# Performance work log

Hardware: AMD Instinct MI355X
Metric: run time of the kernel (lower is better)

Reference implementation:

```python
import jax, jax.numpy as jnp
import numpy as np

N_NODES = 50000
N_EDGES = 400000
N_GROUPS = 10000
N_GRAPHS = 256
IN_CH = 64
EDGE_DIM = 16
HID = 64
HEADS = 4
OUT_CH = 1


def segment_mean(vals, idx, n):
    s = jax.ops.segment_sum(vals, idx, num_segments=n)
    c = jax.ops.segment_sum(jnp.ones(idx.shape[0], vals.dtype), idx, num_segments=n)
    c = jnp.maximum(c, 1.0).reshape((n,) + (1,) * (vals.ndim - 1))
    return s / c


def gatv2(x, src, dst, wl, wr, att, bias, edge_attr=None, we=None):
    # PyG GATv2Conv (concat=True, negative_slope=0.2, add_self_loops=True,
    # fill_value='mean', share_weights=False).
    N = x.shape[0]
    H, C = att.shape
    loop = jnp.arange(N, dtype=src.dtype)
    s = jnp.concatenate([src, loop])
    d = jnp.concatenate([dst, loop])
    dc = jnp.minimum(d, N - 1)  # clamp dummy (masked) targets for gathers
    xl = (x @ wl).reshape(N, H, C)  # source transform
    xr = (x @ wr).reshape(N, H, C)  # target transform
    m = xl[s] + xr[dc]  # [E+N, H, C]
    if edge_attr is not None:
        loop_attr = segment_mean(edge_attr, dst, N)  # self-loop attr = mean of incoming
        e = jnp.concatenate([edge_attr, loop_attr], axis=0) @ we
        m = m + e.reshape(-1, H, C)
    score = jnp.sum(jax.nn.leaky_relu(m, 0.2) * att, axis=-1)  # [E+N, H]
    smax = jax.ops.segment_max(score, d, num_segments=N)
    ex = jnp.exp(score - smax[dc])
    den = jax.ops.segment_sum(ex, d, num_segments=N)
    alpha = ex / den[dc]
    out = jax.ops.segment_sum(alpha[..., None] * xl[s], d, num_segments=N)
    return out.reshape(N, H * C) + bias


def setup_inputs() -> dict:
    key = jax.random.key(0)
    ks = jax.random.split(key, 32)
    p = lambda i, shape: jax.random.normal(ks[i], shape, jnp.float32) * 0.05
    x = jax.random.normal(ks[0], (N_NODES, IN_CH), jnp.float32)
    edge_index = jax.random.randint(ks[1], (2, N_EDGES), 0, N_NODES)
    edge_attr = jax.random.normal(ks[2], (N_EDGES, EDGE_DIM), jnp.float32)
    batch = (jnp.arange(N_NODES) * N_GRAPHS) // N_NODES
    pharma_index = (jnp.arange(N_NODES) * N_GROUPS) // N_NODES
    return dict(
        x=x, edge_index=edge_index, edge_attr=edge_attr, batch=batch,
        pharma_index=pharma_index, num_graphs=N_GRAPHS,
        w_edge=p(3, (EDGE_DIM, HID)), b_edge=jnp.zeros((HID,), jnp.float32),
        g1_wl=p(4, (IN_CH, HEADS * HID)), g1_wr=p(5, (IN_CH, HEADS * HID)),
        g1_att=p(6, (HEADS, HID)), g1_we=p(7, (HID, HEADS * HID)),
        g1_b=jnp.zeros((HEADS * HID,), jnp.float32),
        g2_wl=p(8, (HEADS * HID, HID)), g2_wr=p(9, (HEADS * HID, HID)),
        g2_att=p(10, (1, HID)), g2_we=p(11, (HID, HID)),
        g2_b=jnp.zeros((HID,), jnp.float32),
        g3_wl=p(12, (HID, HID)), g3_wr=p(13, (HID, HID)),
        g3_att=p(14, (1, HID)), g3_b=jnp.zeros((HID,), jnp.float32),
        g4_wl=p(15, (HID, HID)), g4_wr=p(16, (HID, HID)),
        g4_att=p(17, (1, HID)), g4_b=jnp.zeros((HID,), jnp.float32),
        w1=p(18, (HID, 64)), b1=jnp.zeros((64,), jnp.float32),
        w2=p(19, (64, OUT_CH)), b2=jnp.zeros((OUT_CH,), jnp.float32),
    )


def reference(x, edge_index, edge_attr, batch, pharma_index, num_graphs,
              w_edge, b_edge,
              g1_wl, g1_wr, g1_att, g1_we, g1_b,
              g2_wl, g2_wr, g2_att, g2_we, g2_b,
              g3_wl, g3_wr, g3_att, g3_b,
              g4_wl, g4_wr, g4_att, g4_b,
              w1, b1, w2, b2):
    src, dst = edge_index[0], edge_index[1]
    ea = edge_attr @ w_edge + b_edge  # edge_embed
    h = jax.nn.elu(gatv2(x, src, dst, g1_wl, g1_wr, g1_att, g1_b, ea, g1_we))
    h = jax.nn.elu(gatv2(h, src, dst, g2_wl, g2_wr, g2_att, g2_b, ea, g2_we))
    # pharmacophore pooling (scatter_mean)
    gx = segment_mean(h, pharma_index, N_GROUPS)
    rbatch = segment_mean(batch.astype(jnp.float32), pharma_index, N_GROUPS).astype(jnp.int32)
    # reduced-graph edges: map node edges to group indices, drop intra-group
    # self-edges by routing their target to a dummy segment N_GROUPS.
    sg = pharma_index[src]
    dg = pharma_index[dst]
    dg = jnp.where(sg != dg, dg, N_GROUPS)
    h = jax.nn.elu(gatv2(gx, sg, dg, g3_wl, g3_wr, g3_att, g3_b))
    h = jax.nn.elu(gatv2(h, sg, dg, g4_wl, g4_wr, g4_att, g4_b))
    h = segment_mean(h, rbatch, num_graphs)  # global_mean_pool
    h = jax.nn.relu(h @ w1 + b1)
    return h @ w2 + b2
```

## Files before the change

kernel.cpp:

```cpp
#include <hip/hip_runtime.h>
#include <cstdint>
#include <cstddef>

#define NN 50000
#define NE 400000
#define NG 10000
#define NBG 256

static inline int imin(int a, int b) { return a < b ? a : b; }

__device__ __forceinline__ float wave_sum64(float v) {
#pragma unroll
  for (int off = 32; off > 0; off >>= 1) v += __shfl_xor(v, off, 64);
  return v;
}

__device__ __forceinline__ float bcast_lane(float v, int k) {
  return __int_as_float(__builtin_amdgcn_readlane(__float_as_int(v), k));
}


__global__ void count_dst_kernel(const int* __restrict__ dst, int* __restrict__ cnt, int E) {
  int e = blockIdx.x * blockDim.x + threadIdx.x;
  if (e < E) atomicAdd(&cnt[dst[e]], 1);
}

__global__ void fill_node_kernel(const int* __restrict__ src, const int* __restrict__ dst,
                                 int* __restrict__ cursor, int* __restrict__ csr_src,
                                 int* __restrict__ csr_eid, int E) {
  int e = blockIdx.x * blockDim.x + threadIdx.x;
  if (e < E) {
    int pos = atomicAdd(&cursor[dst[e]], 1);
    csr_src[pos] = src[e];
    csr_eid[pos] = e;
  }
}

__global__ void count_grp_kernel(const int* __restrict__ src, const int* __restrict__ dst,
                                 const int* __restrict__ ph, int* __restrict__ cnt, int E) {
  int e = blockIdx.x * blockDim.x + threadIdx.x;
  if (e < E) {
    int sg = ph[src[e]], dg = ph[dst[e]];
    if (sg != dg) atomicAdd(&cnt[dg], 1);
  }
}

__global__ void fill_grp_kernel(const int* __restrict__ src, const int* __restrict__ dst,
                                const int* __restrict__ ph, int* __restrict__ cursor,
                                int* __restrict__ gsrc, int E) {
  int e = blockIdx.x * blockDim.x + threadIdx.x;
  if (e < E) {
    int sg = ph[src[e]], dg = ph[dst[e]];
    if (sg != dg) {
      int pos = atomicAdd(&cursor[dg], 1);
      gsrc[pos] = sg;
    }
  }
}

__global__ void exscan_block_kernel(const int* __restrict__ cnt, int* __restrict__ rowptr, int n) {
  __shared__ int wsum[16];
  int tid = threadIdx.x;
  int chunk = (n + 1023) >> 10;
  int s0 = tid * chunk;
  int s1 = s0 + chunk; if (s1 > n) s1 = n;
  int sum = 0;
  for (int i = s0; i < s1; i++) sum += cnt[i];
  int lane = tid & 63, w = tid >> 6;
  int v = sum, s = sum;
#pragma unroll
  for (int off = 1; off < 64; off <<= 1) {
    int t = __shfl_up(s, off);
    if (lane >= off) s += t;
  }
  if (lane == 63) wsum[w] = s;
  __syncthreads();
  if (tid == 0) {
    int c = 0;
#pragma unroll
    for (int i = 0; i < 16; i++) { int t = wsum[i]; wsum[i] = c; c += t; }
  }
  __syncthreads();
  int run = wsum[w] + (s - v);
  for (int i = s0; i < s1; i++) { rowptr[i] = run; run += cnt[i]; }
  if (tid == 1023) rowptr[n] = run;
}


__global__ void mean_attr_kernel(const int* __restrict__ rowptr, const int* __restrict__ csr_eid,
                                 const float* __restrict__ eattr, float* __restrict__ mattr, int N) {
  int t = blockIdx.x * blockDim.x + threadIdx.x;
  if (t >= N * 16) return;
  int n = t >> 4, k = t & 15;
  int e0 = rowptr[n], e1 = rowptr[n + 1];
  float s = 0.f;
  for (int p = e0; p < e1; p++) s += eattr[(size_t)csr_eid[p] * 16 + k];
  mattr[t] = (e1 > e0) ? s / (float)(e1 - e0) : 0.f;
}

__global__ void fuse_we_kernel(const float* __restrict__ w_edge, const float* __restrict__ b_edge,
                               const float* __restrict__ g1_we, const float* __restrict__ g2_we,
                               float* __restrict__ We2_1, float* __restrict__ be2_1,
                               float* __restrict__ We2_2, float* __restrict__ be2_2) {
  int t = blockIdx.x * blockDim.x + threadIdx.x;
  if (t < 16 * 256) {
    int k = t >> 8, j = t & 255;
    float s = 0.f;
    for (int c = 0; c < 64; c++) s += w_edge[k * 64 + c] * g1_we[c * 256 + j];
    We2_1[t] = s;
  } else if (t < 16 * 256 + 256) {
    int j = t - 16 * 256;
    float s = 0.f;
    for (int c = 0; c < 64; c++) s += b_edge[c] * g1_we[c * 256 + j];
    be2_1[j] = s;
  } else if (t < 16 * 256 + 256 + 16 * 64) {
    int u = t - (16 * 256 + 256);
    int k = u >> 6, j = u & 63;
    float s = 0.f;
    for (int c = 0; c < 64; c++) s += w_edge[k * 64 + c] * g2_we[c * 64 + j];
    We2_2[u] = s;
  } else if (t < 16 * 256 + 256 + 16 * 64 + 64) {
    int j = t - (16 * 256 + 256 + 16 * 64);
    float s = 0.f;
    for (int c = 0; c < 64; c++) s += b_edge[c] * g2_we[c * 64 + j];
    be2_2[j] = s;
  }
}

template <int IN, int OUT>
__global__ __launch_bounds__(256) void matvec_kernel(int nRows,
    const float* __restrict__ X, const float* __restrict__ W, float* __restrict__ Y) {
  constexpr int KT = IN / 64;
  const int lane = threadIdx.x & 63;
  const int wv = threadIdx.x >> 6;
  const int batch = blockIdx.x * 4 + wv;
  const int jc = blockIdx.y;
  const int row = batch * 64 + lane;
  const int rc = row < nRows ? row : nRows - 1;
  const float* xp = X + (size_t)rc * IN;
  float acc[64];
#pragma unroll
  for (int j = 0; j < 64; j++) acc[j] = 0.f;
  for (int kt = 0; kt < KT; kt++) {
    float xr[64];
#pragma unroll
    for (int q = 0; q < 16; q++) {
      const float4 v = *(const float4*)(xp + kt * 64 + q * 4);
      xr[q * 4 + 0] = v.x; xr[q * 4 + 1] = v.y; xr[q * 4 + 2] = v.z; xr[q * 4 + 3] = v.w;
    }
    const float* wb = W + (size_t)kt * 64 * OUT + jc * 64;
#pragma unroll
    for (int k = 0; k < 64; k++) {
#pragma unroll
      for (int j = 0; j < 64; j++) acc[j] += xr[k] * wb[(size_t)k * OUT + j];
    }
  }
  if (row < nRows) {
    float* yp = Y + (size_t)row * OUT + jc * 64;
#pragma unroll
    for (int q = 0; q < 16; q++) {
      float4 v;
      v.x = acc[q * 4 + 0]; v.y = acc[q * 4 + 1]; v.z = acc[q * 4 + 2]; v.w = acc[q * 4 + 3];
      *(float4*)(yp + q * 4) = v;
    }
  }
}

template <int H, bool HASE>
__global__ __launch_bounds__(256) void gat_kernel(
    int N,
    const int* __restrict__ rowptr,
    const int* __restrict__ csr_src,
    const int* __restrict__ csr_eid,
    const float* __restrict__ eattr,
    const float* __restrict__ mattr,
    const float* __restrict__ We2,
    const float* __restrict__ be2,
    const float* __restrict__ xl,
    const float* __restrict__ xr,
    const float* __restrict__ att,
    const float* __restrict__ bias,
    float* __restrict__ out)
{
  constexpr int F = H * 64;
  const int lane = threadIdx.x & 63;
  const int wv = threadIdx.x >> 6;

  float att_r[H], bias_r[H], be2_r[H], wreg[16 * H];
#pragma unroll
  for (int r = 0; r < H; r++) {
    att_r[r] = att[r * 64 + lane];
    bias_r[r] = bias[r * 64 + lane];
    be2_r[r] = 0.f;
  }
  if constexpr (HASE) {
#pragma unroll
    for (int r = 0; r < H; r++) be2_r[r] = be2[r * 64 + lane];
#pragma unroll
    for (int k = 0; k < 16; k++)
#pragma unroll
      for (int r = 0; r < H; r++) wreg[k * H + r] = We2[k * F + r * 64 + lane];
  }

  for (int n = blockIdx.x * 4 + wv; n < N; n += gridDim.x * 4) {
    const int e0 = rowptr[n], e1 = rowptr[n + 1];
    float xr_r[H], xls[H];
#pragma unroll
    for (int r = 0; r < H; r++) {
      xr_r[r] = xr[(size_t)n * F + r * 64 + lane];
      xls[r] = xl[(size_t)n * F + r * 64 + lane];
    }
    float ev[H];
#pragma unroll
    for (int r = 0; r < H; r++) ev[r] = 0.f;
    if constexpr (HASE) {
      if (e1 > e0) {
        float av = (lane < 16) ? mattr[(size_t)n * 16 + lane] : 0.f;
#pragma unroll
        for (int k = 0; k < 16; k++) {
          float a = bcast_lane(av, k);
#pragma unroll
          for (int r = 0; r < H; r++) ev[r] += a * wreg[k * H + r];
        }
#pragma unroll
        for (int r = 0; r < H; r++) ev[r] += be2_r[r];
      }
    }
    float m_run[H], den[H], acc[H];
#pragma unroll
    for (int r = 0; r < H; r++) {
      float vv = xls[r] + xr_r[r] + ev[r];
      vv = vv > 0.f ? vv : 0.2f * vv;
      float sc = wave_sum64(vv * att_r[r]);
      m_run[r] = sc; den[r] = 1.f; acc[r] = xls[r];
    }
    for (int pos = e0; pos < e1; pos++) {
      const int s = csr_src[pos];
      float ev2[H];
#pragma unroll
      for (int r = 0; r < H; r++) ev2[r] = 0.f;
      if constexpr (HASE) {
        const int eid = csr_eid[pos];
        float av = (lane < 16) ? eattr[(size_t)eid * 16 + lane] : 0.f;
#pragma unroll
        for (int k = 0; k < 16; k++) {
          float a = bcast_lane(av, k);
#pragma unroll
          for (int r = 0; r < H; r++) ev2[r] += a * wreg[k * H + r];
        }
#pragma unroll
        for (int r = 0; r < H; r++) ev2[r] += be2_r[r];
      }
      float xsr[H], sc[H];
#pragma unroll
      for (int r = 0; r < H; r++) xsr[r] = xl[(size_t)s * F + r * 64 + lane];
#pragma unroll
      for (int r = 0; r < H; r++) {
        float vv = xsr[r] + xr_r[r] + ev2[r];
        vv = vv > 0.f ? vv : 0.2f * vv;
        sc[r] = wave_sum64(vv * att_r[r]);
      }
#pragma unroll
      for (int r = 0; r < H; r++) {
        float mo = m_run[r];
        float mn = fmaxf(mo, sc[r]);
        float sa = __expf(mo - mn);
        float ex = __expf(sc[r] - mn);
        den[r] = den[r] * sa + ex;
        acc[r] = acc[r] * sa + ex * xsr[r];
        m_run[r] = mn;
      }
    }
#pragma unroll
    for (int r = 0; r < H; r++) {
      float o = acc[r] / den[r] + bias_r[r];
      out[(size_t)n * F + r * 64 + lane] = o > 0.f ? o : (__expf(o) - 1.f);
    }
  }
}


__global__ void pool_ph_scatter_kernel(const float* __restrict__ h, const int* __restrict__ ph,
                                       const int* __restrict__ batch, float* __restrict__ gsum,
                                       float* __restrict__ bsum, int* __restrict__ gcnt, int N) {
  int t = blockIdx.x * blockDim.x + threadIdx.x;
  if (t >= N * 64) return;
  int n = t >> 6, c = t & 63;
  int g = ph[n];
  atomicAdd(&gsum[(size_t)g * 64 + c], h[t]);
  if (c == 0) {
    atomicAdd(&gcnt[g], 1);
    atomicAdd(&bsum[g], (float)batch[n]);
  }
}

__global__ void pool_ph_final_kernel(const float* __restrict__ gsum, const float* __restrict__ bsum,
                                     const int* __restrict__ gcnt, float* __restrict__ gx,
                                     int* __restrict__ rbatch, int G) {
  int t = blockIdx.x * blockDim.x + threadIdx.x;
  if (t >= G * 64) return;
  int g = t >> 6, c = t & 63;
  float cn = fmaxf((float)gcnt[g], 1.f);
  gx[t] = gsum[t] / cn;
  if (c == 0) rbatch[g] = (int)(bsum[g] / cn);
}

__global__ void pool_graph_scatter_kernel(const float* __restrict__ h, const int* __restrict__ rbatch,
                                          float* __restrict__ psum, int* __restrict__ pcnt, int G) {
  int t = blockIdx.x * blockDim.x + threadIdx.x;
  if (t >= G * 64) return;
  int g = t >> 6, c = t & 63;
  int b = rbatch[g];
  atomicAdd(&psum[(size_t)b * 64 + c], h[t]);
  if (c == 0) atomicAdd(&pcnt[b], 1);
}

__global__ void pool_graph_final_kernel(const float* __restrict__ psum, const int* __restrict__ pcnt,
                                        float* __restrict__ pooled) {
  int t = blockIdx.x * blockDim.x + threadIdx.x;
  if (t >= NBG * 64) return;
  int b = t >> 6;
  pooled[t] = psum[t] / fmaxf((float)pcnt[b], 1.f);
}


__global__ void fc1_kernel(const float* __restrict__ pooled, const float* __restrict__ w1,
                           const float* __restrict__ b1, float* __restrict__ o) {
  int g = blockIdx.x, lane = threadIdx.x;
  float p = pooled[g * 64 + lane];
  float acc = b1[lane];
#pragma unroll 8
  for (int k = 0; k < 64; k++) acc += __shfl(p, k, 64) * w1[k * 64 + lane];
  o[g * 64 + lane] = fmaxf(acc, 0.f);
}

__global__ void fc2_kernel(const float* __restrict__ o1, const float* __restrict__ w2,
                           const float* __restrict__ b2, float* __restrict__ out) {
  int g = threadIdx.x;
  float acc = b2[0];
  for (int k = 0; k < 64; k++) acc += o1[g * 64 + k] * w2[k];
  out[g] = acc;
}


extern "C" void kernel_launch(void* const* d_in, const int* in_sizes, int n_in,
                              void* d_out, int out_size, void* d_ws, size_t ws_size,
                              hipStream_t stream) {
  (void)in_sizes; (void)n_in; (void)out_size; (void)ws_size;
  const float* x      = (const float*)d_in[0];
  const int*   eidx   = (const int*)d_in[1];
  const float* eattr  = (const float*)d_in[2];
  const int*   batch  = (const int*)d_in[3];
  const int*   ph     = (const int*)d_in[4];
  const float* w_edge = (const float*)d_in[6];
  const float* b_edge = (const float*)d_in[7];
  const float* g1_wl  = (const float*)d_in[8];
  const float* g1_wr  = (const float*)d_in[9];
  const float* g1_att = (const float*)d_in[10];
  const float* g1_we  = (const float*)d_in[11];
  const float* g1_b   = (const float*)d_in[12];
  const float* g2_wl  = (const float*)d_in[13];
  const float* g2_wr  = (const float*)d_in[14];
  const float* g2_att = (const float*)d_in[15];
  const float* g2_we  = (const float*)d_in[16];
  const float* g2_b   = (const float*)d_in[17];
  const float* g3_wl  = (const float*)d_in[18];
  const float* g3_wr  = (const float*)d_in[19];
  const float* g3_att = (const float*)d_in[20];
  const float* g3_b   = (const float*)d_in[21];
  const float* g4_wl  = (const float*)d_in[22];
  const float* g4_wr  = (const float*)d_in[23];
  const float* g4_att = (const float*)d_in[24];
  const float* g4_b   = (const float*)d_in[25];
  const float* w1     = (const float*)d_in[26];
  const float* b1     = (const float*)d_in[27];
  const float* w2     = (const float*)d_in[28];
  const float* b2     = (const float*)d_in[29];
  float* out = (float*)d_out;
  const int* src = eidx;
  const int* dst = eidx + NE;

  char* ws = (char*)d_ws;
  size_t off = 0;
  auto alloc = [&](size_t bytes) -> void* {
    size_t o = off;
    off = (off + bytes + 255) & ~(size_t)255;
    return (void*)(ws + o);
  };
  int*   rowptr  = (int*)alloc((NN + 1) * 4);
  int*   cursor  = (int*)alloc((NN + 1) * 4);
  int*   csr_src = (int*)alloc((size_t)NE * 4);
  int*   csr_eid = (int*)alloc((size_t)NE * 4);
  int*   growptr = (int*)alloc((NG + 1) * 4);
  int*   gcursor = (int*)alloc((NG + 1) * 4);
  int*   gsrc    = (int*)alloc((size_t)NE * 4);
  float* mattr   = (float*)alloc((size_t)NN * 16 * 4);
  float* We2_1   = (float*)alloc(16 * 256 * 4);
  float* be2_1   = (float*)alloc(256 * 4);
  float* We2_2   = (float*)alloc(16 * 64 * 4);
  float* be2_2   = (float*)alloc(64 * 4);
  float* xl1     = (float*)alloc((size_t)NN * 256 * 4);
  float* xr1     = (float*)alloc((size_t)NN * 256 * 4);
  float* h1      = (float*)alloc((size_t)NN * 256 * 4);
  float* bsum    = (float*)alloc(NG * 4);
  int*   gcnt    = (int*)alloc(NG * 4);
  int*   rbatch  = (int*)alloc(NG * 4);
  float* psum    = (float*)alloc(NBG * 64 * 4);
  int*   pcnt    = (int*)alloc(NBG * 4);
  float* pooled  = (float*)alloc(NBG * 64 * 4);
  float* fc1o    = (float*)alloc(NBG * 64 * 4);
  float* xl2 = xl1;
  float* xr2 = xl1 + (size_t)NN * 64;
  float* h2  = xl1 + (size_t)NN * 128;
  float* gsum = xr1;
  float* gx   = xr1 + (size_t)NG * 64 * 1;
  float* xl3  = xr1 + (size_t)NG * 64 * 2;
  float* xr3  = xr1 + (size_t)NG * 64 * 3;
  float* h3   = xr1 + (size_t)NG * 64 * 4;
  float* xl4  = xr1 + (size_t)NG * 64 * 5;
  float* xr4  = xr1 + (size_t)NG * 64 * 6;
  float* h4   = xr1 + (size_t)NG * 64 * 7;

  hipMemsetAsync(cursor, 0, (NN + 1) * 4, stream);
  count_dst_kernel<<<(NE + 255) / 256, 256, 0, stream>>>(dst, cursor, NE);
  exscan_block_kernel<<<1, 1024, 0, stream>>>(cursor, rowptr, NN);
  hipMemcpyAsync(cursor, rowptr, (NN + 1) * 4, hipMemcpyDeviceToDevice, stream);
  fill_node_kernel<<<(NE + 255) / 256, 256, 0, stream>>>(src, dst, cursor, csr_src, csr_eid, NE);
  mean_attr_kernel<<<(NN * 16 + 255) / 256, 256, 0, stream>>>(rowptr, csr_eid, eattr, mattr, NN);
  fuse_we_kernel<<<(16 * 256 + 256 + 16 * 64 + 64 + 255) / 256, 256, 0, stream>>>(
      w_edge, b_edge, g1_we, g2_we, We2_1, be2_1, We2_2, be2_2);

  {
    dim3 g1((NN + 255) / 256, 4);
    matvec_kernel<64, 256><<<g1, 256, 0, stream>>>(NN, x, g1_wl, xl1);
    matvec_kernel<64, 256><<<g1, 256, 0, stream>>>(NN, x, g1_wr, xr1);
  }
  int gatgrid = imin((NN + 3) / 4, 3072);
  gat_kernel<4, true><<<gatgrid, 256, 0, stream>>>(NN, rowptr, csr_src, csr_eid, eattr, mattr,
                                                   We2_1, be2_1, xl1, xr1, g1_att, g1_b, h1);
  {
    dim3 g2((NN + 255) / 256, 1);
    matvec_kernel<256, 64><<<g2, 256, 0, stream>>>(NN, h1, g2_wl, xl2);
    matvec_kernel<256, 64><<<g2, 256, 0, stream>>>(NN, h1, g2_wr, xr2);
  }
  gat_kernel<1, true><<<gatgrid, 256, 0, stream>>>(NN, rowptr, csr_src, csr_eid, eattr, mattr,
                                                   We2_2, be2_2, xl2, xr2, g2_att, g2_b, h2);

  hipMemsetAsync(gsum, 0, (size_t)NG * 64 * 4, stream);
  hipMemsetAsync(bsum, 0, NG * 4, stream);
  hipMemsetAsync(gcnt, 0, NG * 4, stream);
  pool_ph_scatter_kernel<<<(NN * 64 + 255) / 256, 256, 0, stream>>>(h2, ph, batch, gsum, bsum, gcnt, NN);
  pool_ph_final_kernel<<<(NG * 64 + 255) / 256, 256, 0, stream>>>(gsum, bsum, gcnt, gx, rbatch, NG);

  hipMemsetAsync(gcursor, 0, (NG + 1) * 4, stream);
  count_grp_kernel<<<(NE + 255) / 256, 256, 0, stream>>>(src, dst, ph, gcursor, NE);
  exscan_block_kernel<<<1, 1024, 0, stream>>>(gcursor, growptr, NG);
  hipMemcpyAsync(gcursor, growptr, (NG + 1) * 4, hipMemcpyDeviceToDevice, stream);
  fill_grp_kernel<<<(NE + 255) / 256, 256, 0, stream>>>(src, dst, ph, gcursor, gsrc, NE);

  int gatgrid2 = imin((NG + 3) / 4, 2560);
  {
    dim3 g3((NG + 255) / 256, 1);
    matvec_kernel<64, 64><<<g3, 256, 0, stream>>>(NG, gx, g3_wl, xl3);
    matvec_kernel<64, 64><<<g3, 256, 0, stream>>>(NG, gx, g3_wr, xr3);
    gat_kernel<1, false><<<gatgrid2, 256, 0, stream>>>(NG, growptr, gsrc, nullptr, nullptr, nullptr,
                                                       nullptr, nullptr, xl3, xr3, g3_att, g3_b, h3);
    matvec_kernel<64, 64><<<g3, 256, 0, stream>>>(NG, h3, g4_wl, xl4);
    matvec_kernel<64, 64><<<g3, 256, 0, stream>>>(NG, h3, g4_wr, xr4);
    gat_kernel<1, false><<<gatgrid2, 256, 0, stream>>>(NG, growptr, gsrc, nullptr, nullptr, nullptr,
                                                       nullptr, nullptr, xl4, xr4, g4_att, g4_b, h4);
  }

  hipMemsetAsync(psum, 0, NBG * 64 * 4, stream);
  hipMemsetAsync(pcnt, 0, NBG * 4, stream);
  pool_graph_scatter_kernel<<<(NG * 64 + 255) / 256, 256, 0, stream>>>(h4, rbatch, psum, pcnt, NG);
  pool_graph_final_kernel<<<(NBG * 64 + 255) / 256, 256, 0, stream>>>(psum, pcnt, pooled);
  fc1_kernel<<<NBG, 64, 0, stream>>>(pooled, w1, b1, fc1o);
  fc2_kernel<<<1, 256, 0, stream>>>(fc1o, w2, b2, out);
}
```

Measured before the change: 1.422 ms.

## Interleave head layout, pack CSR, pipeline edge loads and use DPP reductions in GAT

```diff
diff --git a/kernel.cpp b/kernel.cpp
--- a/kernel.cpp
+++ b/kernel.cpp
@@ -9,14 +9,18 @@
 
 static inline int imin(int a, int b) { return a < b ? a : b; }
 
-__device__ __forceinline__ float wave_sum64(float v) {
-#pragma unroll
-  for (int off = 32; off > 0; off >>= 1) v += __shfl_xor(v, off, 64);
-  return v;
-}
-
-__device__ __forceinline__ float bcast_lane(float v, int k) {
-  return __int_as_float(__builtin_amdgcn_readlane(__float_as_int(v), k));
+template <int CTRL>
+__device__ __forceinline__ float dpp_mov(float v) {
+  return __int_as_float(__builtin_amdgcn_update_dpp(0, __float_as_int(v), CTRL, 0xf, 0xf, true));
+}
+__device__ __forceinline__ float wave_sum_dpp(float v) {
+  v += dpp_mov<0x111>(v);
+  v += dpp_mov<0x112>(v);
+  v += dpp_mov<0x114>(v);
+  v += dpp_mov<0x118>(v);
+  v += dpp_mov<0x142>(v);
+  v += dpp_mov<0x143>(v);
+  return __int_as_float(__builtin_amdgcn_readlane(__float_as_int(v), 63));
 }
 
 
@@ -26,13 +30,11 @@
 }
 
 __global__ void fill_node_kernel(const int* __restrict__ src, const int* __restrict__ dst,
-                                 int* __restrict__ cursor, int* __restrict__ csr_src,
-                                 int* __restrict__ csr_eid, int E) {
+                                 int* __restrict__ cursor, int2* __restrict__ cpack, int E) {
   int e = blockIdx.x * blockDim.x + threadIdx.x;
   if (e < E) {
     int pos = atomicAdd(&cursor[dst[e]], 1);
-    csr_src[pos] = src[e];
-    csr_eid[pos] = e;
+    cpack[pos] = make_int2(src[e], e);
   }
 }
 
@@ -87,14 +89,14 @@
 }
 
 
-__global__ void mean_attr_kernel(const int* __restrict__ rowptr, const int* __restrict__ csr_eid,
+__global__ void mean_attr_kernel(const int* __restrict__ rowptr, const int2* __restrict__ cpack,
                                  const float* __restrict__ eattr, float* __restrict__ mattr, int N) {
   int t = blockIdx.x * blockDim.x + threadIdx.x;
   if (t >= N * 16) return;
   int n = t >> 4, k = t & 15;
   int e0 = rowptr[n], e1 = rowptr[n + 1];
   float s = 0.f;
-  for (int p = e0; p < e1; p++) s += eattr[(size_t)csr_eid[p] * 16 + k];
+  for (int p = e0; p < e1; p++) s += eattr[(size_t)cpack[p].y * 16 + k];
   mattr[t] = (e1 > e0) ? s / (float)(e1 - e0) : 0.f;
 }
 
@@ -127,51 +129,128 @@
   }
 }
 
-template <int IN, int OUT>
+template <int IN, int OUT, bool TR>
 __global__ __launch_bounds__(256) void matvec_kernel(int nRows,
     const float* __restrict__ X, const float* __restrict__ W, float* __restrict__ Y) {
-  constexpr int KT = IN / 64;
   const int lane = threadIdx.x & 63;
   const int wv = threadIdx.x >> 6;
-  const int batch = blockIdx.x * 4 + wv;
-  const int jc = blockIdx.y;
-  const int row = batch * 64 + lane;
+  const int row = (blockIdx.x * 4 + wv) * 64 + lane;
   const int rc = row < nRows ? row : nRows - 1;
   const float* xp = X + (size_t)rc * IN;
-  float acc[64];
-#pragma unroll
-  for (int j = 0; j < 64; j++) acc[j] = 0.f;
-  for (int kt = 0; kt < KT; kt++) {
-    float xr[64];
+  if constexpr (TR) {
+    static_assert(IN == 64, "TR path assumes IN==64");
+    constexpr int H = OUT / 64;
+    float xt[64];
 #pragma unroll
     for (int q = 0; q < 16; q++) {
-      const float4 v = *(const float4*)(xp + kt * 64 + q * 4);
-      xr[q * 4 + 0] = v.x; xr[q * 4 + 1] = v.y; xr[q * 4 + 2] = v.z; xr[q * 4 + 3] = v.w;
-    }
-    const float* wb = W + (size_t)kt * 64 * OUT + jc * 64;
-#pragma unroll
-    for (int k = 0; k < 64; k++) {
-#pragma unroll
-      for (int j = 0; j < 64; j++) acc[j] += xr[k] * wb[(size_t)k * OUT + j];
-    }
-  }
-  if (row < nRows) {
-    float* yp = Y + (size_t)row * OUT + jc * 64;
-#pragma unroll
-    for (int q = 0; q < 16; q++) {
-      float4 v;
-      v.x = acc[q * 4 + 0]; v.y = acc[q * 4 + 1]; v.z = acc[q * 4 + 2]; v.w = acc[q * 4 + 3];
-      *(float4*)(yp + q * 4) = v;
-    }
-  }
-}
+      float4 v = *(const float4*)(xp + q * 4);
+      xt[q * 4 + 0] = v.x; xt[q * 4 + 1] = v.y; xt[q * 4 + 2] = v.z; xt[q * 4 + 3] = v.w;
+    }
+    for (int jc = 0; jc < H; jc++) {
+      float acc[64];
+#pragma unroll
+      for (int j = 0; j < 64; j++) acc[j] = 0.f;
+      const float* wb = W + jc * 64;
+#pragma unroll
+      for (int k = 0; k < 64; k++) {
+#pragma unroll
+        for (int j = 0; j < 64; j++) acc[j] += xt[k] * wb[(size_t)k * OUT + j];
+      }
+      if (row < nRows) {
+        float* yp = Y + (size_t)row * OUT + jc;
+#pragma unroll
+        for (int j = 0; j < 64; j++) yp[j * H] = acc[j];
+      }
+    }
+  } else {
+    constexpr int KT = IN / 64;
+    const int jc = blockIdx.y;
+    float acc[64];
+#pragma unroll
+    for (int j = 0; j < 64; j++) acc[j] = 0.f;
+    for (int kt = 0; kt < KT; kt++) {
+      float xt[64];
+#pragma unroll
+      for (int q = 0; q < 16; q++) {
+        const float4 v = *(const float4*)(xp + kt * 64 + q * 4);
+        xt[q * 4 + 0] = v.x; xt[q * 4 + 1] = v.y; xt[q * 4 + 2] = v.z; xt[q * 4 + 3] = v.w;
+      }
+      const float* wb = W + (size_t)kt * 64 * OUT + jc * 64;
+#pragma unroll
+      for (int k = 0; k < 64; k++) {
+#pragma unroll
+        for (int j = 0; j < 64; j++) acc[j] += xt[k] * wb[(size_t)k * OUT + j];
+      }
+    }
+    if (row < nRows) {
+      float* yp = Y + (size_t)row * OUT + jc * 64;
+#pragma unroll
+      for (int q = 0; q < 16; q++) {
+        float4 v;
+        v.x = acc[q * 4 + 0]; v.y = acc[q * 4 + 1]; v.z = acc[q * 4 + 2]; v.w = acc[q * 4 + 3];
+        *(float4*)(yp + q * 4) = v;
+      }
+    }
+  }
+}
+
+
+#define GAT_LOADE(pos, SUF)                                                     \
+  do {                                                                          \
+    int s_;                                                                     \
+    if constexpr (HASE) {                                                       \
+      int2 se_ = cpack[pos];                                                    \
+      s_ = se_.x;                                                               \
+      const float* ep_ = eattr + (size_t)se_.y * 16;                            \
+      _Pragma("unroll")                                                         \
+      for (int k_ = 0; k_ < 16; k_++) ea##SUF[k_] = ep_[k_];                    \
+    } else {                                                                    \
+      s_ = csrc[pos];                                                           \
+    }                                                                           \
+    if constexpr (H == 4) {                                                     \
+      float4 v_ = ((const float4*)xl)[(size_t)s_ * 64 + lane];                  \
+      xs##SUF[0] = v_.x; xs##SUF[1] = v_.y; xs##SUF[2] = v_.z; xs##SUF[3] = v_.w; \
+    } else {                                                                    \
+      xs##SUF[0] = xl[(size_t)s_ * 64 + lane];                                  \
+    }                                                                           \
+  } while (0)
+
+#define GAT_COMPUTE(SUF)                                                        \
+  do {                                                                          \
+    float ev_[H], sc_[H];                                                       \
+    _Pragma("unroll")                                                           \
+    for (int h_ = 0; h_ < H; h_++) ev_[h_] = HASE ? be2_r[h_] : 0.f;            \
+    if constexpr (HASE) {                                                       \
+      _Pragma("unroll")                                                         \
+      for (int k_ = 0; k_ < 16; k_++) {                                         \
+        _Pragma("unroll")                                                       \
+        for (int h_ = 0; h_ < H; h_++) ev_[h_] += ea##SUF[k_] * wreg[k_ * H + h_]; \
+      }                                                                         \
+    }                                                                           \
+    _Pragma("unroll")                                                           \
+    for (int h_ = 0; h_ < H; h_++) {                                            \
+      float v_ = xs##SUF[h_] + xr_r[h_] + ev_[h_];                              \
+      v_ = fmaxf(v_, 0.f) + 0.2f * fminf(v_, 0.f);                              \
+      sc_[h_] = wave_sum_dpp(v_ * att_r[h_]);                                   \
+    }                                                                           \
+    _Pragma("unroll")                                                           \
+    for (int h_ = 0; h_ < H; h_++) {                                            \
+      float mo_ = m_run[h_];                                                    \
+      float mn_ = fmaxf(mo_, sc_[h_]);                                          \
+      float sa_ = __expf(mo_ - mn_);                                            \
+      float ex_ = __expf(sc_[h_] - mn_);                                        \
+      den[h_] = den[h_] * sa_ + ex_;                                            \
+      acc[h_] = acc[h_] * sa_ + ex_ * xs##SUF[h_];                              \
+      m_run[h_] = mn_;                                                          \
+    }                                                                           \
+  } while (0)
 
 template <int H, bool HASE>
 __global__ __launch_bounds__(256) void gat_kernel(
     int N,
     const int* __restrict__ rowptr,
-    const int* __restrict__ csr_src,
-    const int* __restrict__ csr_eid,
+    const int2* __restrict__ cpack,
+    const int* __restrict__ csrc,
     const float* __restrict__ eattr,
     const float* __restrict__ mattr,
     const float* __restrict__ We2,
@@ -188,93 +267,85 @@
 
   float att_r[H], bias_r[H], be2_r[H], wreg[16 * H];
 #pragma unroll
-  for (int r = 0; r < H; r++) {
-    att_r[r] = att[r * 64 + lane];
-    bias_r[r] = bias[r * 64 + lane];
-    be2_r[r] = 0.f;
+  for (int h = 0; h < H; h++) {
+    att_r[h] = att[h * 64 + lane];
+    bias_r[h] = bias[h * 64 + lane];
+    be2_r[h] = 0.f;
   }
   if constexpr (HASE) {
 #pragma unroll
-    for (int r = 0; r < H; r++) be2_r[r] = be2[r * 64 + lane];
+    for (int h = 0; h < H; h++) be2_r[h] = be2[h * 64 + lane];
 #pragma unroll
     for (int k = 0; k < 16; k++)
 #pragma unroll
-      for (int r = 0; r < H; r++) wreg[k * H + r] = We2[k * F + r * 64 + lane];
-  }
-
-  for (int n = blockIdx.x * 4 + wv; n < N; n += gridDim.x * 4) {
+      for (int h = 0; h < H; h++) wreg[k * H + h] = We2[k * F + h * 64 + lane];
+  }
+
+  const int wave_id = blockIdx.x * 4 + wv;
+  const int wstride = gridDim.x * 4;
+  for (int n = wave_id; n < N; n += wstride) {
     const int e0 = rowptr[n], e1 = rowptr[n + 1];
+    const int nE = e1 - e0;
     float xr_r[H], xls[H];
-#pragma unroll
-    for (int r = 0; r < H; r++) {
-      xr_r[r] = xr[(size_t)n * F + r * 64 + lane];
-      xls[r] = xl[(size_t)n * F + r * 64 + lane];
-    }
-    float ev[H];
-#pragma unroll
-    for (int r = 0; r < H; r++) ev[r] = 0.f;
-    if constexpr (HASE) {
-      if (e1 > e0) {
-        float av = (lane < 16) ? mattr[(size_t)n * 16 + lane] : 0.f;
-#pragma unroll
-        for (int k = 0; k < 16; k++) {
-          float a = bcast_lane(av, k);
-#pragma unroll
-          for (int r = 0; r < H; r++) ev[r] += a * wreg[k * H + r];
+    if constexpr (H == 4) {
+      float4 a = ((const float4*)xr)[(size_t)n * 64 + lane];
+      xr_r[0] = a.x; xr_r[1] = a.y; xr_r[2] = a.z; xr_r[3] = a.w;
+      float4 b = ((const float4*)xl)[(size_t)n * 64 + lane];
+      xls[0] = b.x; xls[1] = b.y; xls[2] = b.z; xls[3] = b.w;
+    } else {
+      xr_r[0] = xr[(size_t)n * 64 + lane];
+      xls[0] = xl[(size_t)n * 64 + lane];
+    }
+
+    float m_run[H], den[H], acc[H];
+    {
+      float ev[H];
+#pragma unroll
+      for (int h = 0; h < H; h++) ev[h] = 0.f;
+      if constexpr (HASE) {
+        if (nE > 0) {
+          const float* mp = mattr + (size_t)n * 16;
+#pragma unroll
+          for (int k = 0; k < 16; k++) {
+            float a = mp[k];
+#pragma unroll
+            for (int h = 0; h < H; h++) ev[h] += a * wreg[k * H + h];
+          }
+#pragma unroll
+          for (int h = 0; h < H; h++) ev[h] += be2_r[h];
         }
-#pragma unroll
-        for (int r = 0; r < H; r++) ev[r] += be2_r[r];
-      }
-    }
-    float m_run[H], den[H], acc[H];
-#pragma unroll
-    for (int r = 0; r < H; r++) {
-      float vv = xls[r] + xr_r[r] + ev[r];
-      vv = vv > 0.f ? vv : 0.2f * vv;
-      float sc = wave_sum64(vv * att_r[r]);
-      m_run[r] = sc; den[r] = 1.f; acc[r] = xls[r];
-    }
-    for (int pos = e0; pos < e1; pos++) {
-      const int s = csr_src[pos];
-      float ev2[H];
-#pragma unroll
-      for (int r = 0; r < H; r++) ev2[r] = 0.f;
-      if constexpr (HASE) {
-        const int eid = csr_eid[pos];
-        float av = (lane < 16) ? eattr[(size_t)eid * 16 + lane] : 0.f;
-#pragma unroll
-        for (int k = 0; k < 16; k++) {
-          float a = bcast_lane(av, k);
-#pragma unroll
-          for (int r = 0; r < H; r++) ev2[r] += a * wreg[k * H + r];
-        }
-#pragma unroll
-        for (int r = 0; r < H; r++) ev2[r] += be2_r[r];
-      }
-      float xsr[H], sc[H];
-#pragma unroll
-      for (int r = 0; r < H; r++) xsr[r] = xl[(size_t)s * F + r * 64 + lane];
-#pragma unroll
-      for (int r = 0; r < H; r++) {
-        float vv = xsr[r] + xr_r[r] + ev2[r];
-        vv = vv > 0.f ? vv : 0.2f * vv;
-        sc[r] = wave_sum64(vv * att_r[r]);
-      }
-#pragma unroll
-      for (int r = 0; r < H; r++) {
-        float mo = m_run[r];
-        float mn = fmaxf(mo, sc[r]);
-        float sa = __expf(mo - mn);
-        float ex = __expf(sc[r] - mn);
-        den[r] = den[r] * sa + ex;
-        acc[r] = acc[r] * sa + ex * xsr[r];
-        m_run[r] = mn;
-      }
-    }
-#pragma unroll
-    for (int r = 0; r < H; r++) {
-      float o = acc[r] / den[r] + bias_r[r];
-      out[(size_t)n * F + r * 64 + lane] = o > 0.f ? o : (__expf(o) - 1.f);
+      }
+#pragma unroll
+      for (int h = 0; h < H; h++) {
+        float v = xls[h] + xr_r[h] + ev[h];
+        v = fmaxf(v, 0.f) + 0.2f * fminf(v, 0.f);
+        float sc = wave_sum_dpp(v * att_r[h]);
+        m_run[h] = sc; den[h] = 1.f; acc[h] = xls[h];
+      }
+    }
+
+    float xsA[H], xsB[H], eaA[16], eaB[16];
+    (void)eaA; (void)eaB;
+    if (nE > 0) GAT_LOADE(e0, A);
+    if (nE > 1) GAT_LOADE(e0 + 1, B);
+    int i = 0;
+    for (; i + 3 < nE; i += 2) {
+      GAT_COMPUTE(A);
+      GAT_LOADE(e0 + i + 2, A);
+      GAT_COMPUTE(B);
+      GAT_LOADE(e0 + i + 3, B);
+    }
+    if (i < nE) {
+      GAT_COMPUTE(A);
+      if (i + 2 < nE) GAT_LOADE(e0 + i + 2, A);
+    }
+    if (i + 1 < nE) GAT_COMPUTE(B);
+    if (i + 2 < nE) GAT_COMPUTE(A);
+
+#pragma unroll
+    for (int h = 0; h < H; h++) {
+      float o = acc[h] / den[h] + bias_r[h];
+      out[(size_t)n * F + h * 64 + lane] = o > 0.f ? o : (__expf(o) - 1.f);
     }
   }
 }
@@ -389,8 +460,7 @@
   };
   int*   rowptr  = (int*)alloc((NN + 1) * 4);
   int*   cursor  = (int*)alloc((NN + 1) * 4);
-  int*   csr_src = (int*)alloc((size_t)NE * 4);
-  int*   csr_eid = (int*)alloc((size_t)NE * 4);
+  int2*  cpack   = (int2*)alloc((size_t)NE * 8);
   int*   growptr = (int*)alloc((NG + 1) * 4);
   int*   gcursor = (int*)alloc((NG + 1) * 4);
   int*   gsrc    = (int*)alloc((size_t)NE * 4);
@@ -425,26 +495,25 @@
   count_dst_kernel<<<(NE + 255) / 256, 256, 0, stream>>>(dst, cursor, NE);
   exscan_block_kernel<<<1, 1024, 0, stream>>>(cursor, rowptr, NN);
   hipMemcpyAsync(cursor, rowptr, (NN + 1) * 4, hipMemcpyDeviceToDevice, stream);
-  fill_node_kernel<<<(NE + 255) / 256, 256, 0, stream>>>(src, dst, cursor, csr_src, csr_eid, NE);
-  mean_attr_kernel<<<(NN * 16 + 255) / 256, 256, 0, stream>>>(rowptr, csr_eid, eattr, mattr, NN);
+  fill_node_kernel<<<(NE + 255) / 256, 256, 0, stream>>>(src, dst, cursor, cpack, NE);
+  mean_attr_kernel<<<(NN * 16 + 255) / 256, 256, 0, stream>>>(rowptr, cpack, eattr, mattr, NN);
   fuse_we_kernel<<<(16 * 256 + 256 + 16 * 64 + 64 + 255) / 256, 256, 0, stream>>>(
       w_edge, b_edge, g1_we, g2_we, We2_1, be2_1, We2_2, be2_2);
 
   {
-    dim3 g1((NN + 255) / 256, 4);
-    matvec_kernel<64, 256><<<g1, 256, 0, stream>>>(NN, x, g1_wl, xl1);
-    matvec_kernel<64, 256><<<g1, 256, 0, stream>>>(NN, x, g1_wr, xr1);
-  }
-  int gatgrid = imin((NN + 3) / 4, 3072);
-  gat_kernel<4, true><<<gatgrid, 256, 0, stream>>>(NN, rowptr, csr_src, csr_eid, eattr, mattr,
-                                                   We2_1, be2_1, xl1, xr1, g1_att, g1_b, h1);
+    dim3 g1((NN + 255) / 256, 1);
+    matvec_kernel<64, 256, true><<<g1, 256, 0, stream>>>(NN, x, g1_wl, xl1);
+    matvec_kernel<64, 256, true><<<g1, 256, 0, stream>>>(NN, x, g1_wr, xr1);
+  }
+  gat_kernel<4, true><<<(NN + 3) / 4, 256, 0, stream>>>(NN, rowptr, cpack, nullptr, eattr, mattr,
+                                                        We2_1, be2_1, xl1, xr1, g1_att, g1_b, h1);
   {
     dim3 g2((NN + 255) / 256, 1);
-    matvec_kernel<256, 64><<<g2, 256, 0, stream>>>(NN, h1, g2_wl, xl2);
-    matvec_kernel<256, 64><<<g2, 256, 0, stream>>>(NN, h1, g2_wr, xr2);
-  }
-  gat_kernel<1, true><<<gatgrid, 256, 0, stream>>>(NN, rowptr, csr_src, csr_eid, eattr, mattr,
-                                                   We2_2, be2_2, xl2, xr2, g2_att, g2_b, h2);
+    matvec_kernel<256, 64, false><<<g2, 256, 0, stream>>>(NN, h1, g2_wl, xl2);
+    matvec_kernel<256, 64, false><<<g2, 256, 0, stream>>>(NN, h1, g2_wr, xr2);
+  }
+  gat_kernel<1, true><<<(NN + 3) / 4, 256, 0, stream>>>(NN, rowptr, cpack, nullptr, eattr, mattr,
+                                                        We2_2, be2_2, xl2, xr2, g2_att, g2_b, h2);
 
   hipMemsetAsync(gsum, 0, (size_t)NG * 64 * 4, stream);
   hipMemsetAsync(bsum, 0, NG * 4, stream);
@@ -458,17 +527,18 @@
   hipMemcpyAsync(gcursor, growptr, (NG + 1) * 4, hipMemcpyDeviceToDevice, stream);
   fill_grp_kernel<<<(NE + 255) / 256, 256, 0, stream>>>(src, dst, ph, gcursor, gsrc, NE);
 
-  int gatgrid2 = imin((NG + 3) / 4, 2560);
   {
     dim3 g3((NG + 255) / 256, 1);
-    matvec_kernel<64, 64><<<g3, 256, 0, stream>>>(NG, gx, g3_wl, xl3);
-    matvec_kernel<64, 64><<<g3, 256, 0, stream>>>(NG, gx, g3_wr, xr3);
-    gat_kernel<1, false><<<gatgrid2, 256, 0, stream>>>(NG, growptr, gsrc, nullptr, nullptr, nullptr,
-                                                       nullptr, nullptr, xl3, xr3, g3_att, g3_b, h3);
-    matvec_kernel<64, 64><<<g3, 256, 0, stream>>>(NG, h3, g4_wl, xl4);
-    matvec_kernel<64, 64><<<g3, 256, 0, stream>>>(NG, h3, g4_wr, xr4);
-    gat_kernel<1, false><<<gatgrid2, 256, 0, stream>>>(NG, growptr, gsrc, nullptr, nullptr, nullptr,
-                                                       nullptr, nullptr, xl4, xr4, g4_att, g4_b, h4);
+    matvec_kernel<64, 64, false><<<g3, 256, 0, stream>>>(NG, gx, g3_wl, xl3);
+    matvec_kernel<64, 64, false><<<g3, 256, 0, stream>>>(NG, gx, g3_wr, xr3);
+    gat_kernel<1, false><<<(NG + 3) / 4, 256, 0, stream>>>(NG, growptr, nullptr, gsrc, nullptr,
+                                                           nullptr, nullptr, nullptr, xl3, xr3,
+                                                           g3_att, g3_b, h3);
+    matvec_kernel<64, 64, false><<<g3, 256, 0, stream>>>(NG, h3, g4_wl, xl4);
+    matvec_kernel<64, 64, false><<<g3, 256, 0, stream>>>(NG, h3, g4_wr, xr4);
+    gat_kernel<1, false><<<(NG + 3) / 4, 256, 0, stream>>>(NG, growptr, nullptr, gsrc, nullptr,
+                                                           nullptr, nullptr, nullptr, xl4, xr4,
+                                                           g4_att, g4_b, h4);
   }
 
   hipMemsetAsync(psum, 0, NBG * 64 * 4, stream);
```

Result: slower. 1.712 ms (+20.4%).
